# Kernel optimization log

Hardware: AMD Instinct MI355X
Metric: run time of the kernel (lower is better)

Reference implementation:

```python
import jax, jax.numpy as jnp
import numpy as np

B, IN_DIM, OUT_DIM = 16, 8192, 28672


def setup_inputs() -> dict:
    key = jax.random.key(0)
    k1, k2, k3 = jax.random.split(key, 3)
    x = jax.random.normal(k1, (B, IN_DIM), dtype=jnp.float32)
    # int8 quantized weights stored as int8 (spec'd int32 range [-128,127])
    weight = jax.random.randint(k2, (OUT_DIM, IN_DIM), -128, 128, dtype=jnp.int32).astype(jnp.int8)
    weight_scaler = jax.random.uniform(k3, (OUT_DIM,), dtype=jnp.float32, minval=0.001, maxval=0.02)
    return {"x": x, "weight": weight, "weight_scaler": weight_scaler}


def reference(x, weight, weight_scaler):
    # torch.ops.xla.quantized_matmul per-channel semantics:
    # out[b, o] = sum_i x[b, i] * w[o, i] * scaler[o]
    # Fused dequant-matmul: cast int8 weight to activation dtype, contract, scale.
    w = weight.astype(x.dtype)                      # [out, in]
    out = jnp.einsum("bi,oi->bo", x, w)            # [B, out]
    return out * weight_scaler[None, :]
```

## Files before the change

### kernel.cpp

```cpp
#include <hip/hip_runtime.h>

typedef int v4i __attribute__((ext_vector_type(4)));

#define B_DIM   16
#define IN_DIM  8192
#define OUT_DIM 28672
#define KSTEPS  (IN_DIM / 64)

static __device__ __forceinline__ unsigned pack_lo_bytes(v4i q) {
  unsigned t0 = __builtin_amdgcn_perm((unsigned)q.y, (unsigned)q.x, 0x00000400u);
  unsigned t1 = __builtin_amdgcn_perm((unsigned)q.w, (unsigned)q.z, 0x00000400u);
  return __builtin_amdgcn_perm(t1, t0, 0x05040100u);
}

__global__ __launch_bounds__(256) void xquant_kernel(
    const float* __restrict__ x,
    unsigned char* __restrict__ q1p,
    unsigned char* __restrict__ q2p,
    float* __restrict__ scales)
{
  const int b   = blockIdx.x;
  const int tid = threadIdx.x;
  const float* xr = x + (size_t)b * IN_DIM + tid * 32;

  float v[32];
  float m = 0.0f;
#pragma unroll
  for (int i = 0; i < 8; ++i) {
    float4 f = ((const float4*)xr)[i];
    v[i*4+0] = f.x; v[i*4+1] = f.y; v[i*4+2] = f.z; v[i*4+3] = f.w;
    m = fmaxf(m, fmaxf(fmaxf(fabsf(f.x), fabsf(f.y)), fmaxf(fabsf(f.z), fabsf(f.w))));
  }
#pragma unroll
  for (int off = 32; off >= 1; off >>= 1)
    m = fmaxf(m, __shfl_xor(m, off));
  __shared__ float lmax[4];
  if ((tid & 63) == 0) lmax[tid >> 6] = m;
  __syncthreads();
  m = fmaxf(fmaxf(lmax[0], lmax[1]), fmaxf(lmax[2], lmax[3]));
  m = fmaxf(m, 1e-20f);

  const float s1   = m * (1.0f / 127.0f);
  const float inv1 = 1.0f / s1;
  const float s2   = s1 * (1.0f / 254.0f);
  const float inv2 = 1.0f / s2;
  if (tid == 0) { scales[b] = s1; scales[16 + b] = s2; }

#pragma unroll
  for (int h = 0; h < 2; ++h) {
    const int c = tid * 2 + h;
    unsigned p1[4], p2[4];
#pragma unroll
    for (int d = 0; d < 4; ++d) {
      unsigned a1 = 0, a2 = 0;
#pragma unroll
      for (int j = 0; j < 4; ++j) {
        const float xv = v[h*16 + d*4 + j];
        float q1 = rintf(xv * inv1);
        q1 = fminf(127.0f, fmaxf(-127.0f, q1));
        const float r = fmaf(-s1, q1, xv);
        float q2 = rintf(r * inv2);
        q2 = fminf(127.0f, fmaxf(-127.0f, q2));
        a1 |= ((unsigned)((int)q1 & 0xff)) << (8*j);
        a2 |= ((unsigned)((int)q2 & 0xff)) << (8*j);
      }
      p1[d] = a1; p2[d] = a2;
    }
    const size_t off = (size_t)((c >> 2) * 1024 + (c & 3) * 256 + b * 16);
    *(v4i*)(q1p + off) = (v4i){(int)p1[0], (int)p1[1], (int)p1[2], (int)p1[3]};
    *(v4i*)(q2p + off) = (v4i){(int)p2[0], (int)p2[1], (int)p2[2], (int)p2[3]};
  }
}

__global__ __launch_bounds__(448) void qgemm_kernel(
    const int* __restrict__ w,
    const unsigned char* __restrict__ q1p,
    const unsigned char* __restrict__ q2p,
    const float* __restrict__ scales,
    const float* __restrict__ wscaler,
    float* __restrict__ out)
{
  const int lane = threadIdx.x & 63;
  const int wv   = threadIdx.x >> 6;
  const int col  = lane & 15;
  const int grp  = lane >> 4;
  const int o    = blockIdx.x * 112 + wv * 16 + col;

  const int* wp = w + (size_t)o * IN_DIM + grp * 16;
  const unsigned char* x1p = q1p + lane * 16;
  const unsigned char* x2p = q2p + lane * 16;

  v4i acc1 = {0,0,0,0}, acc2 = {0,0,0,0};

  v4i wb[2][4], xb1[2], xb2[2];
#pragma unroll
  for (int i = 0; i < 2; ++i) {
    const v4i* p = (const v4i*)(wp + i * 64);
    wb[i][0] = p[0]; wb[i][1] = p[1]; wb[i][2] = p[2]; wb[i][3] = p[3];
    xb1[i] = *(const v4i*)(x1p + (size_t)i * 1024);
    xb2[i] = *(const v4i*)(x2p + (size_t)i * 1024);
  }

  for (int kk = 0; kk < KSTEPS; kk += 2) {
#pragma unroll
    for (int i = 0; i < 2; ++i) {
      int kn = kk + i + 2; if (kn > KSTEPS - 1) kn = KSTEPS - 1;
      const v4i* p = (const v4i*)(wp + (size_t)kn * 64);
      v4i nw0 = p[0], nw1 = p[1], nw2 = p[2], nw3 = p[3];
      v4i nx1 = *(const v4i*)(x1p + (size_t)kn * 1024);
      v4i nx2 = *(const v4i*)(x2p + (size_t)kn * 1024);

      v4i bw;
      bw.x = (int)pack_lo_bytes(wb[i][0]);
      bw.y = (int)pack_lo_bytes(wb[i][1]);
      bw.z = (int)pack_lo_bytes(wb[i][2]);
      bw.w = (int)pack_lo_bytes(wb[i][3]);
      acc1 = __builtin_amdgcn_mfma_i32_16x16x64_i8(xb1[i], bw, acc1, 0, 0, 0);
      acc2 = __builtin_amdgcn_mfma_i32_16x16x64_i8(xb2[i], bw, acc2, 0, 0, 0);

      wb[i][0] = nw0; wb[i][1] = nw1; wb[i][2] = nw2; wb[i][3] = nw3;
      xb1[i] = nx1; xb2[i] = nx2;
    }
  }

  const float sc = wscaler[o];
#pragma unroll
  for (int r = 0; r < 4; ++r) {
    const int b = grp * 4 + r;
    const float val = scales[b] * (float)acc1[r] + scales[16 + b] * (float)acc2[r];
    out[(size_t)b * OUT_DIM + o] = val * sc;
  }
}

extern "C" void kernel_launch(void* const* d_in, const int* in_sizes, int n_in,
                              void* d_out, int out_size, void* d_ws, size_t ws_size,
                              hipStream_t stream) {
  const float* x       = (const float*)d_in[0];
  const int*   w       = (const int*)d_in[1];
  const float* wscaler = (const float*)d_in[2];
  float* out = (float*)d_out;

  unsigned char* ws  = (unsigned char*)d_ws;
  unsigned char* q1p = ws;
  unsigned char* q2p = ws + 131072;
  float* scales      = (float*)(ws + 262144);

  xquant_kernel<<<16, 256, 0, stream>>>(x, q1p, q2p, scales);
  qgemm_kernel<<<256, 448, 0, stream>>>(w, q1p, q2p, scales, wscaler, out);
}
```

Measured before the change: 183.3 us.

## Split K across two wave halves per block and reduce partial sums in LDS

The GEMM block doubles to 896 threads. Each group of 7 waves handles half of the input dimension, and the second half's accumulators are summed through shared memory before the epilogue. This doubles the waves in flight for the memory-bound int8 weight stream without adding blocks, so latency should be hidden better. The activation quantization kernel is also rearranged to write packed 4-byte chunks in a different order. The costs are an LDS reduction, a barrier, and half the waves idling during the epilogue.

```diff
diff --git a/kernel.cpp b/kernel.cpp
--- a/kernel.cpp
+++ b/kernel.cpp
@@ -5,7 +5,7 @@
 #define B_DIM   16
 #define IN_DIM  8192
 #define OUT_DIM 28672
-#define KSTEPS  (IN_DIM / 64)
+#define KH      64
 
 static __device__ __forceinline__ unsigned pack_lo_bytes(v4i q) {
   unsigned t0 = __builtin_amdgcn_perm((unsigned)q.y, (unsigned)q.x, 0x00000400u);
@@ -46,16 +46,17 @@
   const float inv2 = 1.0f / s2;
   if (tid == 0) { scales[b] = s1; scales[16 + b] = s2; }
 
+  const int kk = tid >> 1, h2 = tid & 1;
+  unsigned char* b1 = q1p + kk * 1024 + b * 16 + h2 * 8;
+  unsigned char* b2 = q2p + kk * 1024 + b * 16 + h2 * 8;
 #pragma unroll
-  for (int h = 0; h < 2; ++h) {
-    const int c = tid * 2 + h;
-    unsigned p1[4], p2[4];
+  for (int i16 = 0; i16 < 2; ++i16) {
 #pragma unroll
-    for (int d = 0; d < 4; ++d) {
+    for (int grp = 0; grp < 4; ++grp) {
       unsigned a1 = 0, a2 = 0;
 #pragma unroll
       for (int j = 0; j < 4; ++j) {
-        const float xv = v[h*16 + d*4 + j];
+        const float xv = v[i16*16 + grp*4 + j];
         float q1 = rintf(xv * inv1);
         q1 = fminf(127.0f, fmaxf(-127.0f, q1));
         const float r = fmaf(-s1, q1, xv);
@@ -64,15 +65,13 @@
         a1 |= ((unsigned)((int)q1 & 0xff)) << (8*j);
         a2 |= ((unsigned)((int)q2 & 0xff)) << (8*j);
       }
-      p1[d] = a1; p2[d] = a2;
+      *(unsigned*)(b1 + grp*256 + i16*4) = a1;
+      *(unsigned*)(b2 + grp*256 + i16*4) = a2;
     }
-    const size_t off = (size_t)((c >> 2) * 1024 + (c & 3) * 256 + b * 16);
-    *(v4i*)(q1p + off) = (v4i){(int)p1[0], (int)p1[1], (int)p1[2], (int)p1[3]};
-    *(v4i*)(q2p + off) = (v4i){(int)p2[0], (int)p2[1], (int)p2[2], (int)p2[3]};
   }
 }
 
-__global__ __launch_bounds__(448) void qgemm_kernel(
+__global__ __launch_bounds__(896, 4) void qgemm_kernel(
     const int* __restrict__ w,
     const unsigned char* __restrict__ q1p,
     const unsigned char* __restrict__ q2p,
@@ -82,31 +81,36 @@
 {
   const int lane = threadIdx.x & 63;
   const int wv   = threadIdx.x >> 6;
+  const int g    = wv % 7;
+  const int h    = wv / 7;
   const int col  = lane & 15;
   const int grp  = lane >> 4;
-  const int o    = blockIdx.x * 112 + wv * 16 + col;
+  const int o    = blockIdx.x * 112 + g * 16 + col;
 
-  const int* wp = w + (size_t)o * IN_DIM + grp * 16;
-  const unsigned char* x1p = q1p + lane * 16;
-  const unsigned char* x2p = q2p + lane * 16;
+  const char* wpb = (const char*)(w + (size_t)o * IN_DIM + h * (IN_DIM/2)) + grp * 16;
+  const unsigned char* x1p = q1p + h * (KH*1024) + lane * 16;
+  const unsigned char* x2p = q2p + h * (KH*1024) + lane * 16;
 
   v4i acc1 = {0,0,0,0}, acc2 = {0,0,0,0};
 
   v4i wb[2][4], xb1[2], xb2[2];
 #pragma unroll
   for (int i = 0; i < 2; ++i) {
-    const v4i* p = (const v4i*)(wp + i * 64);
-    wb[i][0] = p[0]; wb[i][1] = p[1]; wb[i][2] = p[2]; wb[i][3] = p[3];
+#pragma unroll
+    for (int p = 0; p < 4; ++p)
+      wb[i][p] = *(const v4i*)(wpb + i*256 + p*64);
     xb1[i] = *(const v4i*)(x1p + (size_t)i * 1024);
     xb2[i] = *(const v4i*)(x2p + (size_t)i * 1024);
   }
 
-  for (int kk = 0; kk < KSTEPS; kk += 2) {
+  for (int kk = 0; kk < KH; kk += 2) {
 #pragma unroll
     for (int i = 0; i < 2; ++i) {
-      int kn = kk + i + 2; if (kn > KSTEPS - 1) kn = KSTEPS - 1;
-      const v4i* p = (const v4i*)(wp + (size_t)kn * 64);
-      v4i nw0 = p[0], nw1 = p[1], nw2 = p[2], nw3 = p[3];
+      int kn = kk + i + 2; if (kn > KH - 1) kn = KH - 1;
+      v4i nw0 = *(const v4i*)(wpb + (size_t)kn*256 + 0);
+      v4i nw1 = *(const v4i*)(wpb + (size_t)kn*256 + 64);
+      v4i nw2 = *(const v4i*)(wpb + (size_t)kn*256 + 128);
+      v4i nw3 = *(const v4i*)(wpb + (size_t)kn*256 + 192);
       v4i nx1 = *(const v4i*)(x1p + (size_t)kn * 1024);
       v4i nx2 = *(const v4i*)(x2p + (size_t)kn * 1024);
 
@@ -123,12 +127,19 @@
     }
   }
 
-  const float sc = wscaler[o];
+  __shared__ v4i lds1[7][64], lds2[7][64];
+  if (h == 1) { lds1[g][lane] = acc1; lds2[g][lane] = acc2; }
+  __syncthreads();
+  if (h == 0) {
+    const v4i p1 = lds1[g][lane], p2 = lds2[g][lane];
+    const float sc = wscaler[o];
 #pragma unroll
-  for (int r = 0; r < 4; ++r) {
-    const int b = grp * 4 + r;
-    const float val = scales[b] * (float)acc1[r] + scales[16 + b] * (float)acc2[r];
-    out[(size_t)b * OUT_DIM + o] = val * sc;
+    for (int r = 0; r < 4; ++r) {
+      const int b = grp * 4 + r;
+      const float val = scales[b]      * (float)(acc1[r] + p1[r])
+                      + scales[16 + b] * (float)(acc2[r] + p2[r]);
+      out[(size_t)b * OUT_DIM + o] = val * sc;
+    }
   }
 }
 
@@ -146,5 +157,5 @@
   float* scales      = (float*)(ws + 262144);
 
   xquant_kernel<<<16, 256, 0, stream>>>(x, q1p, q2p, scales);
-  qgemm_kernel<<<256, 448, 0, stream>>>(w, q1p, q2p, scales, wscaler, out);
+  qgemm_kernel<<<256, 896, 0, stream>>>(w, q1p, q2p, scales, wscaler, out);
 }
```

After: 184.4 us. About the same (+0.6%).
